# Performance work log

Measured on AMD Instinct MI355X. Metric: run time of the kernel, lower is better.

The kernel has to match this reference:

```python
import jax, jax.numpy as jnp
import numpy as np

DILATION_DEPTH = 10
N_REPEAT = 5
DILATIONS = [2 ** i for i in range(DILATION_DEPTH)] * N_REPEAT  # 50 layers
N_LAYERS = len(DILATIONS)
N_RES = 32
N_SKIP = 512
N_FEAT = 8
B = 8
T = 8192


def setup_inputs() -> dict:
    key = jax.random.key(0)
    ks = jax.random.split(key, 16)
    s = 0.15  # keep gated activations out of saturation
    return {
        "x": jax.random.normal(ks[0], (B, T, N_FEAT), jnp.float32),
        "w_in": jax.random.normal(ks[1], (N_RES, N_FEAT), jnp.float32) * s,
        "b_in": jax.random.normal(ks[2], (N_RES,), jnp.float32) * s,
        "w_sig": jax.random.normal(ks[3], (N_LAYERS, N_RES, N_RES, 2), jnp.float32) * s,
        "b_sig": jax.random.normal(ks[4], (N_LAYERS, N_RES), jnp.float32) * s,
        "w_tanh": jax.random.normal(ks[5], (N_LAYERS, N_RES, N_RES, 2), jnp.float32) * s,
        "b_tanh": jax.random.normal(ks[6], (N_LAYERS, N_RES), jnp.float32) * s,
        "w_skip": jax.random.normal(ks[7], (N_LAYERS, N_SKIP, N_RES), jnp.float32) * s,
        "b_skip": jax.random.normal(ks[8], (N_LAYERS, N_SKIP), jnp.float32) * s,
        "w_res": jax.random.normal(ks[9], (N_LAYERS, N_RES, N_RES), jnp.float32) * s,
        "b_res": jax.random.normal(ks[10], (N_LAYERS, N_RES), jnp.float32) * s,
        "w_post1": jax.random.normal(ks[11], (N_SKIP, N_SKIP), jnp.float32) * s,
        "b_post1": jax.random.normal(ks[12], (N_SKIP,), jnp.float32) * s,
        "w_post2": jax.random.normal(ks[13], (1, N_SKIP), jnp.float32) * s,
        "b_post2": jax.random.normal(ks[14], (1,), jnp.float32) * s,
    }


def _wavenet_fwd(x, w_in, b_in, w_sig, b_sig, w_tanh, b_tanh,
                 w_skip, b_skip, w_res, b_res, w_post1, b_post1, w_post2, b_post2):
    out_len = x.shape[1] - sum(DILATIONS)  # 3077: final valid length
    # input 1x1 conv, (B,T,F) -> (B,C,T)
    h = jnp.einsum("oc,btc->bot", w_in, x) + b_in[:, None]
    skip_sum = jnp.zeros((x.shape[0], w_skip.shape[1], out_len), x.dtype)
    for i, d in enumerate(DILATIONS):
        pre_s = (jnp.einsum("oc,bct->bot", w_sig[i, :, :, 0], h[:, :, :-d])
                 + jnp.einsum("oc,bct->bot", w_sig[i, :, :, 1], h[:, :, d:])
                 + b_sig[i][:, None])
        pre_t = (jnp.einsum("oc,bct->bot", w_tanh[i, :, :, 0], h[:, :, :-d])
                 + jnp.einsum("oc,bct->bot", w_tanh[i, :, :, 1], h[:, :, d:])
                 + b_tanh[i][:, None])
        g = jax.nn.sigmoid(pre_s) * jnp.tanh(pre_t)
        # skip 1x1 commutes with trailing slice; accumulate sum of sliced skips
        skip_sum = skip_sum + (jnp.einsum("oc,bct->bot", w_skip[i], g[:, :, -out_len:])
                               + b_skip[i][:, None])
        h = (jnp.einsum("oc,bct->bot", w_res[i], g) + b_res[i][:, None]) + h[:, :, d:]
    y = jax.nn.elu(skip_sum)
    y = jnp.einsum("oc,bct->bot", w_post1, y) + b_post1[:, None]
    y = jax.nn.elu(y)
    y = jnp.einsum("oc,bct->bot", w_post2, y) + b_post2[:, None]
    return y  # (B, 1, out_len)


def reference(x, w_in, b_in, w_sig, b_sig, w_tanh, b_tanh,
              w_skip, b_skip, w_res, b_res, w_post1, b_post1, w_post2, b_post2):
    return _wavenet_fwd(x, w_in, b_in, w_sig, b_sig, w_tanh, b_tanh,
                        w_skip, b_skip, w_res, b_res, w_post1, b_post1, w_post2, b_post2)
```

## Files before the change

### kernel.cpp

```cpp
#include <hip/hip_runtime.h>
#include <hip/hip_bf16.h>

#define N_LAYERS 50
#define N_RES 32
#define N_SKIP 512
#define N_FEAT 8
#define BATCH 8
#define T_IN 8192
#define OUT_LEN 3077
#define NCOL (BATCH * OUT_LEN)
#define N_TILES ((NCOL + 127) / 128)

typedef __bf16 bf16x8 __attribute__((ext_vector_type(8)));
typedef float  f32x4  __attribute__((ext_vector_type(4)));

#define SZ_HP    ((size_t)BATCH * T_IN * 32 * 2)
#define OFF_HAH  ((size_t)0)
#define OFF_HAL  (OFF_HAH + SZ_HP)
#define OFF_HBH  (OFF_HAL + SZ_HP)
#define OFF_HBL  (OFF_HBH + SZ_HP)
#define OFF_WGH  (OFF_HBL + SZ_HP)
#define SZ_WG    ((size_t)50 * 64 * 64 * 2)
#define OFF_WGL  (OFF_WGH + SZ_WG)
#define OFF_WRH  (OFF_WGL + SZ_WG)
#define SZ_WR    ((size_t)50 * 32 * 32 * 2)
#define OFF_WRL  (OFF_WRH + SZ_WR)
#define OFF_BG   (OFF_WRL + SZ_WR)
#define SZ_BG    ((size_t)50 * 64 * 4)
#define OFF_AP   (OFF_BG + SZ_BG)
#define SZ_AP    ((size_t)512 * 1600 * 2)
#define OFF_W1P  (OFF_AP + SZ_AP)
#define SZ_W1P   ((size_t)512 * 512 * 2)
#define OFF_BS   (OFF_W1P + SZ_W1P)
#define SZ_BS    ((size_t)2048)
#define OFF_SB   (OFF_BS + SZ_BS)
#define SZ_SB    ((size_t)NCOL * 512 * 2)
#define OFF_GT   (OFF_SB + SZ_SB)
#define SZ_GT    ((size_t)NCOL * 1600 * 2)

__device__ __forceinline__ float eluf(float v) {
    return v > 0.0f ? v : (__expf(v) - 1.0f);
}
__device__ __forceinline__ unsigned short f2bf_bits(float f) {
    __hip_bfloat16 h = __float2bfloat16(f);
    return *(unsigned short*)&h;
}
__device__ __forceinline__ float bfb2f(unsigned short u) {
    return __uint_as_float((unsigned)u << 16);
}
__device__ __forceinline__ void gl_lds16(const void* g, void* l) {
    __builtin_amdgcn_global_load_lds(
        (const __attribute__((address_space(1))) void*)g,
        (__attribute__((address_space(3))) void*)l, 16, 0, 0);
}

__global__ __launch_bounds__(256) void in_conv_kernel(
    const float* __restrict__ x, const float* __restrict__ w_in,
    const float* __restrict__ b_in,
    __hip_bfloat16* __restrict__ h_hi, __hip_bfloat16* __restrict__ h_lo)
{
    int tid = threadIdx.x;
    int t = blockIdx.x * 32 + (tid >> 3);
    int grp = tid & 7;
    int b = blockIdx.y;
    const float* xp = x + ((size_t)b * T_IN + t) * 8;
    float4 v0 = *(const float4*)xp;
    float4 v1 = *(const float4*)(xp + 4);
    float xv[8] = {v0.x, v0.y, v0.z, v0.w, v1.x, v1.y, v1.z, v1.w};
    ushort4 oh, ol;
    unsigned short hb[4], lb[4];
#pragma unroll
    for (int e = 0; e < 4; ++e) {
        int oc = grp * 4 + e;
        float acc = b_in[oc];
#pragma unroll
        for (int f = 0; f < 8; ++f) acc += w_in[oc * 8 + f] * xv[f];
        hb[e] = f2bf_bits(acc);
        lb[e] = f2bf_bits(acc - bfb2f(hb[e]));
    }
    oh.x = hb[0]; oh.y = hb[1]; oh.z = hb[2]; oh.w = hb[3];
    ol.x = lb[0]; ol.y = lb[1]; ol.z = lb[2]; ol.w = lb[3];
    size_t base = ((size_t)b * T_IN + t) * 32 + grp * 4;
    *(ushort4*)(h_hi + base) = oh;
    *(ushort4*)(h_lo + base) = ol;
}

__global__ __launch_bounds__(256) void pack_kernel(
    const float* __restrict__ w_skip, const float* __restrict__ b_skip,
    const float* __restrict__ w_post1,
    const float* __restrict__ w_sig, const float* __restrict__ w_tanh,
    const float* __restrict__ w_res,
    const float* __restrict__ b_sig, const float* __restrict__ b_tanh,
    __hip_bfloat16* __restrict__ Apack, __hip_bfloat16* __restrict__ w1pack,
    __hip_bfloat16* __restrict__ wg_hi, __hip_bfloat16* __restrict__ wg_lo,
    __hip_bfloat16* __restrict__ wr_hi, __hip_bfloat16* __restrict__ wr_lo,
    float* __restrict__ bgate, float* __restrict__ bsum)
{
    int tid = blockIdx.x * 256 + threadIdx.x;
    {
        int m = tid / 1600;
        int r = tid - m * 1600;
        int i = r >> 5, c = r & 31;
        Apack[tid] = __float2bfloat16(w_skip[((size_t)i * 512 + m) * 32 + c]);
    }
    if (tid < 512 * 512) w1pack[tid] = __float2bfloat16(w_post1[tid]);
    if (tid < 50 * 64 * 64) {
        int l = tid >> 12;
        int rem = tid & 4095;
        int row = rem >> 6, k = rem & 63;
        int c = row >> 1, f = row & 1;
        int tap = k >> 5, ci = k & 31;
        const float* src = f ? w_tanh : w_sig;
        float v = src[(((size_t)l * 32 + c) * 32 + ci) * 2 + tap];
        unsigned short h = f2bf_bits(v);
        wg_hi[tid] = __float2bfloat16(v);
        wg_lo[tid] = __float2bfloat16(v - bfb2f(h));
    }
    if (tid < 50 * 1024) {
        float v = w_res[tid];
        unsigned short h = f2bf_bits(v);
        wr_hi[tid] = __float2bfloat16(v);
        wr_lo[tid] = __float2bfloat16(v - bfb2f(h));
    }
    if (tid < 50 * 64) {
        int l = tid >> 6, row = tid & 63;
        bgate[tid] = (row & 1) ? b_tanh[l * 32 + (row >> 1)] : b_sig[l * 32 + (row >> 1)];
    }
    if (tid < 512) {
        float s = 0.0f;
        for (int l = 0; l < N_LAYERS; ++l) s += b_skip[l * 512 + tid];
        bsum[tid] = s;
    }
}

template <int S>
__global__ __launch_bounds__(256, 4) void group_kernel(
    const __hip_bfloat16* __restrict__ hi_in, const __hip_bfloat16* __restrict__ lo_in,
    __hip_bfloat16* __restrict__ hi_out, __hip_bfloat16* __restrict__ lo_out,
    __hip_bfloat16* __restrict__ Gt,
    const __hip_bfloat16* __restrict__ wg_hi_all, const __hip_bfloat16* __restrict__ wg_lo_all,
    const __hip_bfloat16* __restrict__ wr_hi_all, const __hip_bfloat16* __restrict__ wr_lo_all,
    const float* __restrict__ bg_all, const float* __restrict__ br_all,
    int l0, int L_in, int n_ut)
{
    __shared__ __align__(16) char lds[4][128 * 80];
    const int tid = threadIdx.x;
    const int lane = tid & 63;
    const int wave = tid >> 6;
    const int q = lane >> 4, r = lane & 15;
    const int c0 = wave * 32;

    int bid = blockIdx.x;
    int u_t = bid % n_ut;
    int rest = bid / n_ut;
    int p = rest % S;
    int b = rest / S;
    int u0 = u_t * 96;
    int u_last = (L_in - 1 - p) / S;

    bf16x8 aI[2];
    {
        union { bf16x8 v; unsigned short u[8]; } t0, t1;
#pragma unroll
        for (int e = 0; e < 8; ++e) { t0.u[e] = 0; t1.u[e] = 0; }
        int j0 = r - 8 * q;
        int j1 = r + 16 - 8 * q;
        if (j0 >= 0 && j0 < 8) t0.u[j0] = 0x3F80;
        if (j1 >= 0 && j1 < 8) t1.u[j1] = 0x3F80;
        aI[0] = t0.v; aI[1] = t1.v;
    }

    bf16x8 pfh[4], pfl[4];
#pragma unroll
    for (int i = 0; i < 4; ++i) {
        int off = (16 * i + r) * 64 + q * 8;
        pfh[i] = *(const bf16x8*)(wg_hi_all + (size_t)l0 * 4096 + off);
        pfl[i] = *(const bf16x8*)(wg_lo_all + (size_t)l0 * 4096 + off);
    }

    {
        int row = tid >> 1, seg = tid & 1;
        int u = u0 + row; if (u > u_last) u = u_last;
        size_t gb = ((size_t)b * L_in + (size_t)u * S + p) * 32 + seg * 16;
        int lb = row * 80 + seg * 32;
        uint4 a0 = *(const uint4*)(hi_in + gb);
        uint4 a1 = *(const uint4*)(hi_in + gb + 8);
        uint4 c0v = *(const uint4*)(lo_in + gb);
        uint4 c1v = *(const uint4*)(lo_in + gb + 8);
        *(uint4*)(lds[0] + lb) = a0; *(uint4*)(lds[0] + lb + 16) = a1;
        *(uint4*)(lds[1] + lb) = c0v; *(uint4*)(lds[1] + lb + 16) = c1v;
    }
    __syncthreads();

    bf16x8 gstash[5][2];

    int cur = 0;
#pragma unroll
    for (int l = 0; l < 5; ++l) {
        const int d = 1 << l;
        const int lg = l0 + l;
        const int L_out = L_in - S * ((2 << l) - 1);
        const int v_out = 129 - (2 << l);
        const char* xh = lds[cur];
        const char* xl = lds[cur + 1];
        char* yh = lds[2 - cur];
        char* yl = lds[3 - cur];

        const __hip_bfloat16* wg_hi = wg_hi_all + (size_t)lg * 4096;
        const __hip_bfloat16* wg_lo = wg_lo_all + (size_t)lg * 4096;
        float4 bgv[4];
#pragma unroll
        for (int i = 0; i < 4; ++i) bgv[i] = *(const float4*)(bg_all + lg * 64 + 16 * i + 4 * q);

        f32x4 acc[4][2] = {};
#pragma unroll
        for (int ks = 0; ks < 2; ++ks) {
            bf16x8 afh[4], afl[4];
            if (ks == 0) {
#pragma unroll
                for (int i = 0; i < 4; ++i) { afh[i] = pfh[i]; afl[i] = pfl[i]; }
            } else {
#pragma unroll
                for (int i = 0; i < 4; ++i) {
                    int off = (16 * i + r) * 64 + 32 + q * 8;
                    afh[i] = *(const bf16x8*)(wg_hi + off);
                    afl[i] = *(const bf16x8*)(wg_lo + off);
                }
            }
#pragma unroll
            for (int jj = 0; jj < 2; ++jj) {
                int cn = c0 + 16 * jj + r;
                int rowk = cn;
                if (ks) { rowk = cn + d; if (rowk > 127) rowk = 127; }
                bf16x8 bhi = *(const bf16x8*)(xh + rowk * 80 + q * 16);
                bf16x8 blo = *(const bf16x8*)(xl + rowk * 80 + q * 16);
#pragma unroll
                for (int i = 0; i < 4; ++i) {
                    acc[i][jj] = __builtin_amdgcn_mfma_f32_16x16x32_bf16(afh[i], bhi, acc[i][jj], 0, 0, 0);
                    acc[i][jj] = __builtin_amdgcn_mfma_f32_16x16x32_bf16(afh[i], blo, acc[i][jj], 0, 0, 0);
                    acc[i][jj] = __builtin_amdgcn_mfma_f32_16x16x32_bf16(afl[i], bhi, acc[i][jj], 0, 0, 0);
                }
            }
        }

#pragma unroll
        for (int i = 0; i < 4; ++i) {
#pragma unroll
            for (int jj = 0; jj < 2; ++jj) {
                int cn = c0 + 16 * jj + r;
                float ps0 = acc[i][jj][0] + bgv[i].x;
                float pt0 = acc[i][jj][1] + bgv[i].y;
                float ps1 = acc[i][jj][2] + bgv[i].z;
                float pt1 = acc[i][jj][3] + bgv[i].w;
                float g0 = __builtin_amdgcn_rcpf(1.0f + __expf(-ps0)) *
                           (1.0f - 2.0f * __builtin_amdgcn_rcpf(__expf(2.0f * pt0) + 1.0f));
                float g1 = __builtin_amdgcn_rcpf(1.0f + __expf(-ps1)) *
                           (1.0f - 2.0f * __builtin_amdgcn_rcpf(__expf(2.0f * pt1) + 1.0f));
                *(unsigned int*)(yh + cn * 80 + 16 * i + 4 * q) =
                    (unsigned)f2bf_bits(g0) | ((unsigned)f2bf_bits(g1) << 16);
            }
        }

        const __hip_bfloat16* wr_hi = wr_hi_all + (size_t)lg * 1024;
        const __hip_bfloat16* wr_lo = wr_lo_all + (size_t)lg * 1024;
        bf16x8 arh[2], arl[2];
#pragma unroll
        for (int i = 0; i < 2; ++i) {
            int off = (16 * i + r) * 32 + q * 8;
            arh[i] = *(const bf16x8*)(wr_hi + off);
            arl[i] = *(const bf16x8*)(wr_lo + off);
        }
        f32x4 racc[2][2] = {};
#pragma unroll
        for (int jj = 0; jj < 2; ++jj) {
            int cn = c0 + 16 * jj + r;
            bf16x8 ghi = *(const bf16x8*)(yh + cn * 80 + q * 16);
            gstash[l][jj] = ghi;
            int r1 = cn + d; if (r1 > 127) r1 = 127;
            bf16x8 x1h = *(const bf16x8*)(xh + r1 * 80 + q * 16);
            bf16x8 x1l = *(const bf16x8*)(xl + r1 * 80 + q * 16);
#pragma unroll
            for (int i = 0; i < 2; ++i) {
                racc[i][jj] = __builtin_amdgcn_mfma_f32_16x16x32_bf16(arh[i], ghi, racc[i][jj], 0, 0, 0);
                racc[i][jj] = __builtin_amdgcn_mfma_f32_16x16x32_bf16(arl[i], ghi, racc[i][jj], 0, 0, 0);
                racc[i][jj] = __builtin_amdgcn_mfma_f32_16x16x32_bf16(aI[i], x1h, racc[i][jj], 0, 0, 0);
                racc[i][jj] = __builtin_amdgcn_mfma_f32_16x16x32_bf16(aI[i], x1l, racc[i][jj], 0, 0, 0);
            }
        }

#pragma unroll
        for (int jj = 0; jj < 2; ++jj) {
            int cn = c0 + 16 * jj + r;
            int t = (u0 + cn) * S + p;
            bool wr_global = (l == 4) && (cn < v_out) && (t < L_out);
#pragma unroll
            for (int i = 0; i < 2; ++i) {
                int ch = 16 * i + 4 * q;
                float4 bb = *(const float4*)(br_all + lg * 32 + ch);
                float o0 = racc[i][jj][0] + bb.x;
                float o1 = racc[i][jj][1] + bb.y;
                float o2 = racc[i][jj][2] + bb.z;
                float o3 = racc[i][jj][3] + bb.w;
                ushort4 oh, ol;
                oh.x = f2bf_bits(o0); ol.x = f2bf_bits(o0 - bfb2f(oh.x));
                oh.y = f2bf_bits(o1); ol.y = f2bf_bits(o1 - bfb2f(oh.y));
                oh.z = f2bf_bits(o2); ol.z = f2bf_bits(o2 - bfb2f(oh.z));
                oh.w = f2bf_bits(o3); ol.w = f2bf_bits(o3 - bfb2f(oh.w));
                if (l == 4) {
                    if (wr_global) {
                        size_t base = ((size_t)b * L_out + t) * 32 + ch;
                        *(ushort4*)(hi_out + base) = oh;
                        *(ushort4*)(lo_out + base) = ol;
                    }
                } else {
                    int off = cn * 80 + ch * 2;
                    *(ushort4*)(yh + off) = oh;
                    *(ushort4*)(yl + off) = ol;
                }
            }
        }
        if (l < 4) {
#pragma unroll
            for (int i = 0; i < 4; ++i) {
                int off = (16 * i + r) * 64 + q * 8;
                pfh[i] = *(const bf16x8*)(wg_hi_all + (size_t)(lg + 1) * 4096 + off);
                pfl[i] = *(const bf16x8*)(wg_lo_all + (size_t)(lg + 1) * 4096 + off);
            }
            __syncthreads();
        }
        cur = 2 - cur;
    }

#pragma unroll
    for (int l = 0; l < 5; ++l) {
        const int lg = l0 + l;
        const int L_out_l = L_in - S * ((2 << l) - 1);
        const int v_out_l = 129 - (2 << l);
        const int ws_l = L_out_l - OUT_LEN;
#pragma unroll
        for (int jj = 0; jj < 2; ++jj) {
            int cn = c0 + 16 * jj + r;
            int t = (u0 + cn) * S + p;
            if (cn < v_out_l && t >= ws_l && t < L_out_l) {
                size_t n = (size_t)b * OUT_LEN + (t - ws_l);
                *(bf16x8*)(Gt + n * 1600 + (size_t)lg * 32 + q * 8) = gstash[l][jj];
            }
        }
    }
}

template <int MODE>
__global__ __launch_bounds__(512) void mfma_gemm_kernel(
    const __hip_bfloat16* __restrict__ A, int lda,
    const __hip_bfloat16* __restrict__ B, int ldb,
    const float* __restrict__ bias, void* __restrict__ Cout,
    const float* __restrict__ w2, float* __restrict__ outp, int K)
{
    int id = blockIdx.x;
    int j = id >> 3;
    int m0 = (j & 1) * 256;
    int nt = (id & 7) + 8 * (j >> 1);
    if (nt >= N_TILES) return;
    int n0 = nt * 128;

    __shared__ __align__(16) char As[256 * 128];
    __shared__ __align__(16) char Bs[128 * 128];
    int tid = threadIdx.x;
    int lane = tid & 63, wave = tid >> 6;
    int wm = (wave & 3) * 64, wn = (wave >> 2) * 64;
    int q = lane >> 4, r = lane & 15;

    f32x4 acc[4][4] = {};

    for (int k0 = 0; k0 < K; k0 += 64) {
        __syncthreads();
#pragma unroll
        for (int i = 0; i < 4; ++i) {
            int li = i * 512 + tid;
            int row = li >> 3, ch = li & 7;
            int cs = (ch ^ (row & 7)) * 8;
            gl_lds16(A + (size_t)(m0 + row) * lda + k0 + cs, As + li * 16);
        }
#pragma unroll
        for (int i = 0; i < 2; ++i) {
            int li = i * 512 + tid;
            int row = li >> 3, ch = li & 7;
            int cs = (ch ^ (row & 7)) * 8;
            int gn = n0 + row; if (gn > NCOL - 1) gn = NCOL - 1;
            gl_lds16(B + (size_t)gn * ldb + k0 + cs, Bs + li * 16);
        }
        __syncthreads();
#pragma unroll
        for (int ks = 0; ks < 2; ++ks) {
            bf16x8 af[4], bfr[4];
#pragma unroll
            for (int s = 0; s < 4; ++s) {
                int m = wm + s * 16 + r;
                int cg = ks * 4 + q;
                af[s]  = *(const bf16x8*)(As + m * 128 + ((cg ^ (m & 7)) * 16));
                int n = wn + s * 16 + r;
                bfr[s] = *(const bf16x8*)(Bs + n * 128 + ((cg ^ (n & 7)) * 16));
            }
#pragma unroll
            for (int i = 0; i < 4; ++i)
#pragma unroll
                for (int jx = 0; jx < 4; ++jx)
                    acc[i][jx] = __builtin_amdgcn_mfma_f32_16x16x32_bf16(
                        af[i], bfr[jx], acc[i][jx], 0, 0, 0);
        }
    }

    if (MODE == 0) {
        __hip_bfloat16* Sb = (__hip_bfloat16*)Cout;
#pragma unroll
        for (int jx = 0; jx < 4; ++jx) {
            int n = n0 + wn + jx * 16 + r;
            if (n >= NCOL) continue;
#pragma unroll
            for (int i = 0; i < 4; ++i) {
                int mb = m0 + wm + i * 16 + q * 4;
                float4 bs = *(const float4*)(bias + mb);
                ushort4 u;
                u.x = f2bf_bits(eluf(acc[i][jx][0] + bs.x));
                u.y = f2bf_bits(eluf(acc[i][jx][1] + bs.y));
                u.z = f2bf_bits(eluf(acc[i][jx][2] + bs.z));
                u.w = f2bf_bits(eluf(acc[i][jx][3] + bs.w));
                *(ushort4*)(Sb + (size_t)n * 512 + mb) = u;
            }
        }
    } else {
        float part[4] = {0.0f, 0.0f, 0.0f, 0.0f};
#pragma unroll
        for (int i = 0; i < 4; ++i) {
            int mb = m0 + wm + i * 16 + q * 4;
            float4 bs = *(const float4*)(bias + mb);
            float4 wv = *(const float4*)(w2 + mb);
#pragma unroll
            for (int jx = 0; jx < 4; ++jx) {
                part[jx] += wv.x * eluf(acc[i][jx][0] + bs.x);
                part[jx] += wv.y * eluf(acc[i][jx][1] + bs.y);
                part[jx] += wv.z * eluf(acc[i][jx][2] + bs.z);
                part[jx] += wv.w * eluf(acc[i][jx][3] + bs.w);
            }
        }
#pragma unroll
        for (int jx = 0; jx < 4; ++jx) {
            float v = part[jx];
            v += __shfl_xor(v, 16, 64);
            v += __shfl_xor(v, 32, 64);
            int n = n0 + wn + jx * 16 + r;
            if (q == 0 && n < NCOL) atomicAdd(outp + n, v);
        }
    }
}

__global__ __launch_bounds__(256) void init_out_kernel(
    const float* __restrict__ b2, float* __restrict__ out, int N)
{
    int n = blockIdx.x * 256 + threadIdx.x;
    if (n < N) out[n] = b2[0];
}

extern "C" void kernel_launch(void* const* d_in, const int* in_sizes, int n_in,
                              void* d_out, int out_size, void* d_ws, size_t ws_size,
                              hipStream_t stream)
{
    const float* x      = (const float*)d_in[0];
    const float* w_in   = (const float*)d_in[1];
    const float* b_in   = (const float*)d_in[2];
    const float* w_sig  = (const float*)d_in[3];
    const float* b_sig  = (const float*)d_in[4];
    const float* w_tanh = (const float*)d_in[5];
    const float* b_tanh = (const float*)d_in[6];
    const float* w_skip = (const float*)d_in[7];
    const float* b_skip = (const float*)d_in[8];
    const float* w_res  = (const float*)d_in[9];
    const float* b_res  = (const float*)d_in[10];
    const float* w_post1 = (const float*)d_in[11];
    const float* b_post1 = (const float*)d_in[12];
    const float* w_post2 = (const float*)d_in[13];
    const float* b_post2 = (const float*)d_in[14];
    float* out = (float*)d_out;

    char* ws = (char*)d_ws;
    __hip_bfloat16* hAh = (__hip_bfloat16*)(ws + OFF_HAH);
    __hip_bfloat16* hAl = (__hip_bfloat16*)(ws + OFF_HAL);
    __hip_bfloat16* hBh = (__hip_bfloat16*)(ws + OFF_HBH);
    __hip_bfloat16* hBl = (__hip_bfloat16*)(ws + OFF_HBL);
    __hip_bfloat16* wgh = (__hip_bfloat16*)(ws + OFF_WGH);
    __hip_bfloat16* wgl = (__hip_bfloat16*)(ws + OFF_WGL);
    __hip_bfloat16* wrh = (__hip_bfloat16*)(ws + OFF_WRH);
    __hip_bfloat16* wrl = (__hip_bfloat16*)(ws + OFF_WRL);
    float* bgate = (float*)(ws + OFF_BG);
    __hip_bfloat16* Apack  = (__hip_bfloat16*)(ws + OFF_AP);
    __hip_bfloat16* w1pack = (__hip_bfloat16*)(ws + OFF_W1P);
    float* bsum = (float*)(ws + OFF_BS);
    __hip_bfloat16* Sb = (__hip_bfloat16*)(ws + OFF_SB);
    __hip_bfloat16* Gt = (__hip_bfloat16*)(ws + OFF_GT);

    in_conv_kernel<<<dim3(T_IN / 32, BATCH), 256, 0, stream>>>(x, w_in, b_in, hAh, hAl);
    pack_kernel<<<dim3(512 * 1600 / 256), 256, 0, stream>>>(
        w_skip, b_skip, w_post1, w_sig, w_tanh, w_res, b_sig, b_tanh,
        Apack, w1pack, wgh, wgl, wrh, wrl, bgate, bsum);

    int L = T_IN;
    __hip_bfloat16 *cih = hAh, *cil = hAl, *coh = hBh, *col_ = hBl;
    for (int rep = 0; rep < 5; ++rep) {
        {
            int out_len = L - 31;
            int n_ut = (out_len + 95) / 96;
            group_kernel<1><<<dim3(BATCH * n_ut), 256, 0, stream>>>(
                cih, cil, coh, col_, Gt, wgh, wgl, wrh, wrl, bgate, b_res,
                rep * 10, L, n_ut);
            L = out_len;
            __hip_bfloat16* t1 = cih; cih = coh; coh = t1;
            __hip_bfloat16* t2 = cil; cil = col_; col_ = t2;
        }
        {
            int U = (L + 31) / 32;
            int out_u = U - 31; if (out_u < 1) out_u = 1;
            int n_ut = (out_u + 95) / 96;
            group_kernel<32><<<dim3(BATCH * 32 * n_ut), 256, 0, stream>>>(
                cih, cil, coh, col_, Gt, wgh, wgl, wrh, wrl, bgate, b_res,
                rep * 10 + 5, L, n_ut);
            L = L - 992;
            __hip_bfloat16* t1 = cih; cih = coh; coh = t1;
            __hip_bfloat16* t2 = cil; cil = col_; col_ = t2;
        }
    }

    mfma_gemm_kernel<0><<<dim3(400), 512, 0, stream>>>(
        Apack, 1600, Gt, 1600, bsum, (void*)Sb, nullptr, nullptr, 1600);
    init_out_kernel<<<dim3((NCOL + 255) / 256), 256, 0, stream>>>(b_post2, out, NCOL);
    mfma_gemm_kernel<1><<<dim3(400), 512, 0, stream>>>(
        w1pack, 512, Sb, 512, b_post1, nullptr, w_post2, out, 512);
}
```

Measured before the change: 526.2 us.

## Prefetch next GEMM K-tile into registers while computing current tile

Replaces the direct global-to-LDS loads in the post-net GEMM with register-staged software pipelining: the next K-slice of A and B is loaded into registers before the MFMA loop on the current slice, then written to LDS afterwards. This is meant to hide global memory latency behind MFMA work instead of stalling at a barrier on each K step. It also changes the thread-to-row mapping for the LDS fill in the residual-stack kernel so consecutive threads read consecutive rows. The cost is higher register pressure from the six uint4 prefetch registers and extra LDS store instructions.

```diff
diff --git a/kernel.cpp b/kernel.cpp
--- a/kernel.cpp
+++ b/kernel.cpp
@@ -48,11 +48,6 @@
 __device__ __forceinline__ float bfb2f(unsigned short u) {
     return __uint_as_float((unsigned)u << 16);
 }
-__device__ __forceinline__ void gl_lds16(const void* g, void* l) {
-    __builtin_amdgcn_global_load_lds(
-        (const __attribute__((address_space(1))) void*)g,
-        (__attribute__((address_space(3))) void*)l, 16, 0, 0);
-}
 
 __global__ __launch_bounds__(256) void in_conv_kernel(
     const float* __restrict__ x, const float* __restrict__ w_in,
@@ -179,7 +174,7 @@
     }
 
     {
-        int row = tid >> 1, seg = tid & 1;
+        int row = tid & 127, seg = tid >> 7;
         int u = u0 + row; if (u > u_last) u = u_last;
         size_t gb = ((size_t)b * L_in + (size_t)u * S + p) * 32 + seg * 16;
         int lb = row * 80 + seg * 32;
@@ -370,26 +365,45 @@
     int wm = (wave & 3) * 64, wn = (wave >> 2) * 64;
     int q = lane >> 4, r = lane & 15;
 
+    int arow[4], acs[4], brow[2], bcs[2];
+#pragma unroll
+    for (int i = 0; i < 4; ++i) {
+        int li = i * 512 + tid;
+        arow[i] = li >> 3; acs[i] = ((li & 7) ^ (arow[i] & 7)) * 8;
+    }
+#pragma unroll
+    for (int i = 0; i < 2; ++i) {
+        int li = i * 512 + tid;
+        int row = li >> 3;
+        int gn = n0 + row; if (gn > NCOL - 1) gn = NCOL - 1;
+        brow[i] = gn; bcs[i] = ((li & 7) ^ (row & 7)) * 8;
+    }
+
     f32x4 acc[4][4] = {};
+    uint4 pa[4], pb[2];
+
+#pragma unroll
+    for (int i = 0; i < 4; ++i)
+        pa[i] = *(const uint4*)(A + (size_t)(m0 + arow[i]) * lda + acs[i]);
+#pragma unroll
+    for (int i = 0; i < 2; ++i)
+        pb[i] = *(const uint4*)(B + (size_t)brow[i] * ldb + bcs[i]);
+#pragma unroll
+    for (int i = 0; i < 4; ++i) *(uint4*)(As + (i * 512 + tid) * 16) = pa[i];
+#pragma unroll
+    for (int i = 0; i < 2; ++i) *(uint4*)(Bs + (i * 512 + tid) * 16) = pb[i];
+    __syncthreads();
 
     for (int k0 = 0; k0 < K; k0 += 64) {
-        __syncthreads();
-#pragma unroll
-        for (int i = 0; i < 4; ++i) {
-            int li = i * 512 + tid;
-            int row = li >> 3, ch = li & 7;
-            int cs = (ch ^ (row & 7)) * 8;
-            gl_lds16(A + (size_t)(m0 + row) * lda + k0 + cs, As + li * 16);
-        }
-#pragma unroll
-        for (int i = 0; i < 2; ++i) {
-            int li = i * 512 + tid;
-            int row = li >> 3, ch = li & 7;
-            int cs = (ch ^ (row & 7)) * 8;
-            int gn = n0 + row; if (gn > NCOL - 1) gn = NCOL - 1;
-            gl_lds16(B + (size_t)gn * ldb + k0 + cs, Bs + li * 16);
-        }
-        __syncthreads();
+        bool more = (k0 + 64 < K);
+        if (more) {
+#pragma unroll
+            for (int i = 0; i < 4; ++i)
+                pa[i] = *(const uint4*)(A + (size_t)(m0 + arow[i]) * lda + k0 + 64 + acs[i]);
+#pragma unroll
+            for (int i = 0; i < 2; ++i)
+                pb[i] = *(const uint4*)(B + (size_t)brow[i] * ldb + k0 + 64 + bcs[i]);
+        }
 #pragma unroll
         for (int ks = 0; ks < 2; ++ks) {
             bf16x8 af[4], bfr[4];
@@ -407,6 +421,14 @@
                 for (int jx = 0; jx < 4; ++jx)
                     acc[i][jx] = __builtin_amdgcn_mfma_f32_16x16x32_bf16(
                         af[i], bfr[jx], acc[i][jx], 0, 0, 0);
+        }
+        if (more) {
+            __syncthreads();
+#pragma unroll
+            for (int i = 0; i < 4; ++i) *(uint4*)(As + (i * 512 + tid) * 16) = pa[i];
+#pragma unroll
+            for (int i = 0; i < 2; ++i) *(uint4*)(Bs + (i * 512 + tid) * 16) = pb[i];
+            __syncthreads();
         }
     }
 
```

After: 695.6 us. 1.32x slower.
